# Kernel tuning notes

Measured on AMD Instinct MI355X. Metric: run time of the kernel, lower is better.

The kernel has to match this reference:

```python
import jax, jax.numpy as jnp
import numpy as np

CIN = 256
WINDOWS = (2, 4, 6)
LN_EPS = 1e-5


def _conv1x1(x, w, b):
    # x: (N,C,H,W), w: (O,C), b: (O,)
    return jnp.einsum('nchw,oc->nohw', x, w) + b[None, :, None, None]


def _pos_encoding(C, H, W):
    # Faithful to SinCosPositionalEncoding2D (incl. its w-major flatten + raw view)
    gw, gh = jnp.meshgrid(jnp.arange(W, dtype=jnp.float32),
                          jnp.arange(H, dtype=jnp.float32), indexing='ij')
    pd = C // 4
    omega = 1.0 / (10000.0 ** (jnp.arange(pd, dtype=jnp.float32) / pd))
    ow = gw.reshape(-1)[:, None] * omega[None, :]
    oh = gh.reshape(-1)[:, None] * omega[None, :]
    pe = jnp.concatenate([jnp.sin(ow), jnp.cos(ow), jnp.sin(oh), jnp.cos(oh)], axis=1)  # (W*H, C)
    return pe.reshape(1, C, H, W)  # raw row-major reinterpret, matching torch .view


def _unfold(x, kh, kw, sh, sw):
    # torch F.unfold semantics: (N,C,H,W) -> (N, C*kh*kw, L), L row-major over (oh, ow)
    N, C, H, W = x.shape
    oh = (H - kh) // sh + 1
    ow = (W - kw) // sw + 1
    ih = (jnp.arange(oh) * sh)[:, None] + jnp.arange(kh)[None, :]  # (oh,kh)
    iw = (jnp.arange(ow) * sw)[:, None] + jnp.arange(kw)[None, :]  # (ow,kw)
    p = x[:, :, ih[:, None, :, None], iw[None, :, None, :]]       # (N,C,oh,ow,kh,kw)
    return jnp.transpose(p, (0, 1, 4, 5, 2, 3)).reshape(N, C * kh * kw, oh * ow)


def _fold(p, H, W, kh, kw, sh, sw):
    # torch F.fold semantics: overlap-add scatter back to (N,C,H,W)
    N = p.shape[0]
    C = p.shape[1] // (kh * kw)
    oh = (H - kh) // sh + 1
    ow = (W - kw) // sw + 1
    p = jnp.transpose(p.reshape(N, C, kh, kw, oh, ow), (0, 1, 4, 5, 2, 3))  # (N,C,oh,ow,kh,kw)
    ih = (jnp.arange(oh) * sh)[:, None] + jnp.arange(kh)[None, :]
    iw = (jnp.arange(ow) * sw)[:, None] + jnp.arange(kw)[None, :]
    out = jnp.zeros((N, C, H, W), p.dtype)
    return out.at[:, :, ih[:, None, :, None], iw[None, :, None, :]].add(p)


def _psa(x, ch_wv_w, ch_wv_b, ch_wq_w, ch_wq_b, ch_wz_w, ch_wz_b, ln_g, ln_b,
         sp_wv_w, sp_wv_b, sp_wq_w, sp_wq_b):
    # Polarized Self-Attention (parallel), input (N,C,H',W')
    N, C, Hh, Ww = x.shape
    C2 = C // 2
    HW = Hh * Ww
    # channel-only branch
    wv = _conv1x1(x, ch_wv_w, ch_wv_b).reshape(N, C2, HW)
    wq = jax.nn.softmax(_conv1x1(x, ch_wq_w, ch_wq_b).reshape(N, HW), axis=-1)
    z = jnp.einsum('ncl,nl->nc', wv, wq)                       # (N, C2)
    wz = jnp.einsum('nc,oc->no', z, ch_wz_w) + ch_wz_b         # (N, C)
    m = wz.mean(-1, keepdims=True)
    v = ((wz - m) ** 2).mean(-1, keepdims=True)
    ch_w = jax.nn.sigmoid((wz - m) / jnp.sqrt(v + LN_EPS) * ln_g + ln_b)
    out_ch = x * ch_w[:, :, None, None]
    # spatial-only branch
    sv = _conv1x1(x, sp_wv_w, sp_wv_b).reshape(N, C2, HW)
    sq = jax.nn.softmax(_conv1x1(x, sp_wq_w, sp_wq_b).mean(axis=(2, 3)), axis=-1)  # (N,C2)
    sp_w = jax.nn.sigmoid(jnp.einsum('nc,ncl->nl', sq, sv)).reshape(N, 1, Hh, Ww)
    return out_ch + x * sp_w


def _forward(x, w_exp, b_exp, w_res, b_res, w_fus, b_fus,
             ch_wv_w, ch_wv_b, ch_wq_w, ch_wq_b, ch_wz_w, ch_wz_b, ln_g, ln_b,
             sp_wv_w, sp_wv_b, sp_wq_w, sp_wq_b):
    N, C, H, W = x.shape
    expx = _conv1x1(x, w_exp, b_exp)                 # (N, 3C, H, W)
    branches = jnp.split(expx, len(WINDOWS), axis=1)
    pos = _pos_encoding(C, H, W)
    outs = []
    for i, win in enumerate(WINDOWS):
        sh, sw = H // win, W // win
        kh, kw = sh + H % win, sw + W % win
        K = kh * kw
        u = _unfold(branches[i], kh, kw, sh, sw).reshape(N, C, win * win, K)
        pu = _unfold(pos, kh, kw, sh, sw).reshape(1, C, win * win, K)
        a = _psa(u + pu, ch_wv_w, ch_wv_b, ch_wq_w, ch_wq_b, ch_wz_w, ch_wz_b,
                 ln_g, ln_b, sp_wv_w, sp_wv_b, sp_wq_w, sp_wq_b)
        a = a.reshape(N, C * K, win * win)           # raw view, matching torch
        cnt = _fold(jnp.ones_like(a), H, W, kh, kw, sh, sw)
        f = _fold(a, H, W, kh, kw, sh, sw) / cnt
        outs.append(f)
    out = _conv1x1(jnp.concatenate(outs, axis=1) + expx, w_res, b_res) + x
    return _conv1x1(out, w_fus, b_fus)


def setup_inputs() -> dict:
    key = jax.random.key(0)
    ks = jax.random.split(key, 10)
    C, C2 = CIN, CIN // 2
    s = 0.02
    nrm = lambda k, shp: jax.random.normal(k, shp, jnp.float32) * s
    return {
        'x': jax.random.normal(ks[0], (8, C, 64, 64), jnp.float32),
        'w_exp': nrm(ks[1], (3 * C, C)), 'b_exp': jnp.zeros((3 * C,), jnp.float32),
        'w_res': nrm(ks[2], (C, 3 * C)), 'b_res': jnp.zeros((C,), jnp.float32),
        'w_fus': nrm(ks[3], (C, C)), 'b_fus': jnp.zeros((C,), jnp.float32),
        'ch_wv_w': nrm(ks[4], (C2, C)), 'ch_wv_b': jnp.zeros((C2,), jnp.float32),
        'ch_wq_w': nrm(ks[5], (1, C)), 'ch_wq_b': jnp.zeros((1,), jnp.float32),
        'ch_wz_w': nrm(ks[6], (C, C2)), 'ch_wz_b': jnp.zeros((C,), jnp.float32),
        'ln_g': jnp.ones((C,), jnp.float32), 'ln_b': jnp.zeros((C,), jnp.float32),
        'sp_wv_w': nrm(ks[7], (C2, C)), 'sp_wv_b': jnp.zeros((C2,), jnp.float32),
        'sp_wq_w': nrm(ks[8], (C2, C)), 'sp_wq_b': jnp.zeros((C2,), jnp.float32),
    }


def reference(x, w_exp, b_exp, w_res, b_res, w_fus, b_fus,
              ch_wv_w, ch_wv_b, ch_wq_w, ch_wq_b, ch_wz_w, ch_wz_b, ln_g, ln_b,
              sp_wv_w, sp_wv_b, sp_wq_w, sp_wq_b):
    return _forward(x, w_exp, b_exp, w_res, b_res, w_fus, b_fus,
                    ch_wv_w, ch_wv_b, ch_wq_w, ch_wq_b, ch_wz_w, ch_wz_b, ln_g, ln_b,
                    sp_wv_w, sp_wv_b, sp_wq_w, sp_wq_b)
```

## Files before the change

kernel.cpp:

```cpp
#include <hip/hip_runtime.h>
#include <cstddef>
#include <cstdint>


#define HW 4096
typedef unsigned short ushort_t;
typedef __attribute__((ext_vector_type(8))) short bf16x8;
typedef __attribute__((ext_vector_type(4))) float floatx4;

#define FMA4(acc, s, v) { acc.x = fmaf((s), (v).x, acc.x); acc.y = fmaf((s), (v).y, acc.y); \
                          acc.z = fmaf((s), (v).z, acc.z); acc.w = fmaf((s), (v).w, acc.w); }
#define SHRED4(v) { v.x += __shfl_down(v.x, 16, 64); v.y += __shfl_down(v.y, 16, 64); \
                    v.z += __shfl_down(v.z, 16, 64); v.w += __shfl_down(v.w, 16, 64); \
                    v.x += __shfl_down(v.x, 32, 64); v.y += __shfl_down(v.y, 32, 64); \
                    v.z += __shfl_down(v.z, 32, 64); v.w += __shfl_down(v.w, 32, 64); }
#define ADD4(a, b) { a.x += (b).x; a.y += (b).y; a.z += (b).z; a.w += (b).w; }

__device__ __forceinline__ ushort_t f2bf(float f) {
    unsigned u = __float_as_uint(f);
    u += 0x7FFF + ((u >> 16) & 1);
    return (ushort_t)(u >> 16);
}
__device__ __forceinline__ float bf2f(ushort_t h) {
    return __uint_as_float(((unsigned)h) << 16);
}

__device__ __forceinline__ int cnt1f(int y, int sh, int kh, int win) {
    int t = y - kh + sh;
    int lo = t > 0 ? t / sh : 0;
    int hi = min(win - 1, y / sh);
    return hi - lo + 1;
}

__device__ __forceinline__ float posval(int f) {
    int row = f >> 8, col = f & 255;
    int a = row >> 6, b = row & 63;
    int g = col >> 6, k = col & 63;
    float omega = expf(-(float)k * (9.2103403719761836f / 64.f));
    float arg = (g < 2 ? (float)a : (float)b) * omega;
    return (g & 1) ? cosf(arg) : sinf(arg);
}

__global__ __launch_bounds__(256) void prep_all(
    const float* __restrict__ x, const float* __restrict__ W_exp,
    const float* __restrict__ b_exp, const float* __restrict__ wq,
    const float* __restrict__ wq_b, const float* __restrict__ W_fus,
    const float* __restrict__ W_res, const float* __restrict__ b_res,
    const float* __restrict__ b_fus, const float* __restrict__ sp_wq_w,
    const float* __restrict__ ch_wv_w, const float* __restrict__ ch_wz_w,
    float* __restrict__ pos, float* __restrict__ posT,
    ushort_t* __restrict__ xbT, ushort_t* __restrict__ wexpb,
    float* __restrict__ g, float* __restrict__ c0out,
    ushort_t* __restrict__ Wcat, float* __restrict__ biasc,
    float* __restrict__ zeroreg,
    float* __restrict__ W_expT, float* __restrict__ swqT,
    float* __restrict__ chvT, float* __restrict__ chzT,
    float* __restrict__ xpa, float* __restrict__ xp6,
    float* __restrict__ ppa, float* __restrict__ pp6)
{
    __shared__ float smf[1184];
    __shared__ float wred[8];
    int b = blockIdx.x, tid = threadIdx.x;
    if (b < 4096) {
        int idx = b * 256 + tid;
        float pv = posval(idx);
        pos[idx] = pv;
        int p2 = idx >> 8, c2 = idx & 255;
        posT[idx] = posval(c2 * 4096 + p2);
        int p = ((b & 15) << 8) + tid;
        int y = p >> 6, xx = p & 63;
        float cf = (float)(cnt1f(y, 10, 14, 6) * cnt1f(xx, 10, 14, 6));
        float s1 = pv, s2 = cf * pv;
        #pragma unroll
        for (int d = 32; d; d >>= 1) {
            s1 += __shfl_down(s1, d, 64);
            s2 += __shfl_down(s2, d, 64);
        }
        if ((tid & 63) == 0) { wred[tid >> 6] = s1; wred[4 + (tid >> 6)] = s2; }
        __syncthreads();
        if (tid == 0) {
            int slot = (b & 15) * 256 + (b >> 4);
            ppa[slot] = wred[0] + wred[1] + wred[2] + wred[3];
            pp6[slot] = wred[4] + wred[5] + wred[6] + wred[7];
        }
    } else if (b < 12288) {
        int v = b - 4096;
        int p0 = (v & 127) * 32, c0 = ((v >> 7) & 7) * 32, n = v >> 10;
        int cc = tid >> 3, p4 = (tid & 7) * 4;
        const float* src = x + (((size_t)(n * 256 + c0 + cc)) << 12) + p0 + p4;
        float4 vv = *(const float4*)src;
        int pg = p0 + p4;
        int y = pg >> 6, xx = pg & 63;
        float cy = (float)cnt1f(y, 10, 14, 6);
        float s6 = cy * ((float)cnt1f(xx, 10, 14, 6) * vv.x
                       + (float)cnt1f(xx + 1, 10, 14, 6) * vv.y
                       + (float)cnt1f(xx + 2, 10, 14, 6) * vv.z
                       + (float)cnt1f(xx + 3, 10, 14, 6) * vv.w);
        float s = vv.x + vv.y + vv.z + vv.w;
        #pragma unroll
        for (int d = 4; d; d >>= 1) {
            s += __shfl_down(s, d, 8);
            s6 += __shfl_down(s6, d, 8);
        }
        if ((tid & 7) == 0) {
            int pblk = v & 127;
            xpa[pblk * 2048 + n * 256 + c0 + cc] = s;
            xp6[pblk * 2048 + n * 256 + c0 + cc] = s6;
        }
        smf[cc * 37 + p4] = vv.x; smf[cc * 37 + p4 + 1] = vv.y;
        smf[cc * 37 + p4 + 2] = vv.z; smf[cc * 37 + p4 + 3] = vv.w;
        __syncthreads();
        int pp = tid >> 3, c4 = (tid & 7) * 4;
        unsigned lo = (unsigned)f2bf(smf[c4 * 37 + pp]) | ((unsigned)f2bf(smf[(c4 + 1) * 37 + pp]) << 16);
        unsigned hi = (unsigned)f2bf(smf[(c4 + 2) * 37 + pp]) | ((unsigned)f2bf(smf[(c4 + 3) * 37 + pp]) << 16);
        *(uint2*)&xbT[(((size_t)(n << 12)) + p0 + pp) * 256 + c0 + c4] = make_uint2(lo, hi);
    } else if (b < 13056) {
        int i = (b - 12288) * 256 + tid;
        wexpb[i] = f2bf(W_exp[i]);
    } else if (b < 13059) {
        int i = b - 13056;
        float* wql = smf;
        float* red = smf + 256;
        wql[tid] = wq[tid];
        red[tid] = wq[tid] * b_exp[i * 256 + tid];
        __syncthreads();
        const float* Wb = W_exp + ((size_t)(i * 256)) * 256 + tid;
        float acc = 0.f;
        #pragma unroll 8
        for (int oc = 0; oc < 256; ++oc) acc = fmaf(wql[oc], Wb[(size_t)oc * 256], acc);
        g[i * 256 + tid] = acc;
        for (int s = 128; s > 0; s >>= 1) { if (tid < s) red[tid] += red[tid + s]; __syncthreads(); }
        if (tid == 0) c0out[i] = red[0] + wq_b[0];
    } else if (b < 13827) {
        int v = b - 13059;
        int o = v & 255, jb = v >> 8;
        float* wrow = smf;
        float* red = smf + 256;
        wrow[tid] = W_fus[o * 256 + tid];
        __syncthreads();
        int j = jb * 256 + tid;
        float acc = 0.f;
        #pragma unroll 8
        for (int c = 0; c < 256; ++c) acc = fmaf(wrow[c], W_res[(size_t)c * 768 + j], acc);
        Wcat[o * 1024 + 256 + j] = f2bf(acc);
        if (jb == 0) {
            Wcat[o * 1024 + tid] = f2bf(wrow[tid]);
            red[tid] = wrow[tid] * b_res[tid];
            __syncthreads();
            for (int s = 128; s > 0; s >>= 1) { if (tid < s) red[tid] += red[tid + s]; __syncthreads(); }
            if (tid == 0) biasc[o] = red[0] + b_fus[o];
        }
    } else if (b < 13875) {
        int i = (b - 13827) * 256 + tid;
        zeroreg[i] = 0.f;
    } else if (b < 14643) {
        int idx = (b - 13875) * 256 + tid;
        W_expT[(idx & 255) * 768 + (idx >> 8)] = W_exp[idx];
    } else if (b < 14771) {
        int idx = (b - 14643) * 256 + tid;
        swqT[(idx & 255) * 128 + (idx >> 8)] = sp_wq_w[idx];
    } else if (b < 14899) {
        int idx = (b - 14771) * 256 + tid;
        chvT[(idx & 255) * 128 + (idx >> 8)] = ch_wv_w[idx];
    } else {
        int idx = (b - 14899) * 256 + tid;
        chzT[(idx & 127) * 256 + (idx >> 7)] = ch_wz_w[idx];
    }
}

__global__ __launch_bounds__(512) void qdot_ubar(
    const float* __restrict__ x, const float* __restrict__ pos,
    const float* __restrict__ g, const float* __restrict__ c0in,
    const float* __restrict__ wq, float* __restrict__ qdot,
    const float* __restrict__ b_exp,
    const float* __restrict__ xpa, const float* __restrict__ xp6,
    const float* __restrict__ ppa, const float* __restrict__ pp6,
    const float* __restrict__ W_expT, float* __restrict__ ubar,
    float* __restrict__ qpm, float* __restrict__ qpz)
{
    int blk = blockIdx.x, tid = threadIdx.x;
    if (blk < 512) {
        int n = blk >> 6;
        int pq = tid & 15, cg = tid >> 4;
        int pb = blk & 63;
        int p = pb * 64 + pq * 4;
        __shared__ float gl[768];
        __shared__ float wql[256];
        __shared__ float4 wp[8][16][4];
        for (int k = tid; k < 768; k += 512) gl[k] = g[k];
        if (tid < 256) wql[tid] = wq[tid];
        __syncthreads();
        const float* xp = x + (((size_t)n) << 20) + p;
        const float* pp = pos + p;
        float4 a0 = make_float4(0.f, 0.f, 0.f, 0.f), a1 = a0, a2 = a0, ap = a0;
        #pragma unroll
        for (int c = cg * 8; c < cg * 8 + 8; ++c) {
            float4 xv = *(const float4*)(xp + ((size_t)c << 12));
            float4 pv = *(const float4*)(pp + ((size_t)c << 12));
            FMA4(a0, gl[c], xv);
            FMA4(a1, gl[256 + c], xv);
            FMA4(a2, gl[512 + c], xv);
            FMA4(ap, wql[c], pv);
        }
        SHRED4(a0); SHRED4(a1); SHRED4(a2); SHRED4(ap);
        int lane = tid & 63, w = tid >> 6;
        if (lane < 16) {
            wp[w][lane][0] = a0; wp[w][lane][1] = a1;
            wp[w][lane][2] = a2; wp[w][lane][3] = ap;
        }
        __syncthreads();
        if (tid < 16) {
            float4 s0 = make_float4(0.f, 0.f, 0.f, 0.f), s1 = s0, s2 = s0, sp = s0;
            #pragma unroll
            for (int w2 = 0; w2 < 8; ++w2) {
                ADD4(s0, wp[w2][tid][0]); ADD4(s1, wp[w2][tid][1]);
                ADD4(s2, wp[w2][tid][2]); ADD4(sp, wp[w2][tid][3]);
            }
            float c00 = c0in[0], c01 = c0in[1], c02 = c0in[2];
            float4 va, vb, vc;
            va.x = s0.x + sp.x + c00; va.y = s0.y + sp.y + c00;
            va.z = s0.z + sp.z + c00; va.w = s0.w + sp.w + c00;
            vb.x = s1.x + sp.x + c01; vb.y = s1.y + sp.y + c01;
            vb.z = s1.z + sp.z + c01; vb.w = s1.w + sp.w + c01;
            vc.x = s2.x + sp.x + c02; vc.y = s2.y + sp.y + c02;
            vc.z = s2.z + sp.z + c02; vc.w = s2.w + sp.w + c02;
            *(float4*)&qdot[((0 * 8 + n) << 12) + p] = va;
            *(float4*)&qdot[((1 * 8 + n) << 12) + p] = vb;
            *(float4*)&qdot[((2 * 8 + n) << 12) + p] = vc;
            int y = p >> 6, xx = p & 63;
            #pragma unroll
            for (int i = 0; i < 3; ++i) {
                int win = 2 * (i + 1), sh = 64 / win, kh = sh + 64 % win;
                float4 v = (i == 0) ? va : (i == 1) ? vb : vc;
                float cy = (float)cnt1f(y, sh, kh, win);
                float cf0 = cy * (float)cnt1f(xx, sh, kh, win);
                float cf1 = cy * (float)cnt1f(xx + 1, sh, kh, win);
                float cf2 = cy * (float)cnt1f(xx + 2, sh, kh, win);
                float cf3 = cy * (float)cnt1f(xx + 3, sh, kh, win);
                float m = fmaxf(fmaxf(v.x, v.y), fmaxf(v.z, v.w));
                #pragma unroll
                for (int d = 8; d; d >>= 1) m = fmaxf(m, __shfl_down(m, d, 16));
                m = __shfl(m, 0, 16);
                float z = cf0 * expf(v.x - m) + cf1 * expf(v.y - m)
                        + cf2 * expf(v.z - m) + cf3 * expf(v.w - m);
                #pragma unroll
                for (int d = 8; d; d >>= 1) z += __shfl_down(z, d, 16);
                if (tid == 0) {
                    int bidx = (i * 8 + n) * 64 + pb;
                    qpm[bidx] = m; qpz[bidx] = z;
                }
            }
        }
    } else {
        int v = blk - 512;
        int i = v >> 3, n = v & 7;
        __shared__ float xbl[256];
        if (tid < 256) {
            const float* xp_ = (i < 2) ? xpa : xp6;
            float s = 0.f;
            #pragma unroll 8
            for (int k = 0; k < 128; ++k) s += xp_[k * 2048 + n * 256 + tid];
            xbl[tid] = s;
        }
        __syncthreads();
        if (tid < 256) {
            const float* pp_ = (i < 2) ? ppa : pp6;
            float pb = 0.f;
            #pragma unroll
            for (int k = 0; k < 16; ++k) pb += pp_[k * 256 + tid];
            int win = 2 * (i + 1), sh = 64 / win, kh = sh + 64 % win;
            float Li = (float)(win * win * kh * kh);
            float acc = b_exp[i * 256 + tid] * Li + pb;
            const float* Wc = W_expT + i * 256 + tid;
            #pragma unroll 8
            for (int j = 0; j < 256; ++j) acc = fmaf(Wc[(size_t)j * 768], xbl[j], acc);
            ubar[(i * 8 + n) * 256 + tid] = acc;
        }
    }
}

__global__ __launch_bounds__(1024) void pass_b_h(
    const float* __restrict__ ubar_raw,
    const float* __restrict__ swqT, const float* __restrict__ sp_wq_b,
    const float* __restrict__ sp_wv_w, const float* __restrict__ sp_wv_b,
    const float* __restrict__ W_exp, const float* __restrict__ b_exp,
    const float* __restrict__ qpm, const float* __restrict__ qpz,
    float* __restrict__ Mn, float* __restrict__ invZn,
    float* __restrict__ w_eff, float* __restrict__ h, float* __restrict__ btot)
{
    int i = blockIdx.x, n = blockIdx.y, tid = threadIdx.x;
    int b = i * 8 + n;
    int win = 2 * (i + 1), sh = 64 / win, kh = sh + 64 % win;
    float invL = 1.f / (float)(win * win * kh * kh);
    __shared__ float ub[256];
    __shared__ float spq[128];
    __shared__ float we[256];
    __shared__ float ps[1024];
    __shared__ float red[256];
    if (tid < 64) {
        float mp = qpm[b * 64 + tid];
        float zp = qpz[b * 64 + tid];
        float mm = mp;
        #pragma unroll
        for (int d = 32; d; d >>= 1) mm = fmaxf(mm, __shfl_down(mm, d, 64));
        float M = __shfl(mm, 0, 64);
        float zz = zp * expf(mp - M);
        #pragma unroll
        for (int d = 32; d; d >>= 1) zz += __shfl_down(zz, d, 64);
        if (tid == 0) { Mn[b] = M; invZn[b] = 1.f / zz; }
    }
    if (tid < 256) ub[tid] = ubar_raw[b * 256 + tid] * invL;
    __syncthreads();
    {
        int q = tid & 127, s8 = tid >> 7;
        float a = 0.f;
        #pragma unroll 8
        for (int c = s8 * 32; c < s8 * 32 + 32; ++c) a = fmaf(swqT[c * 128 + q], ub[c], a);
        ps[tid] = a;
    }
    __syncthreads();
    float sl = 0.f;
    if (tid < 128) {
        float a = sp_wq_b[tid];
        #pragma unroll
        for (int k = 0; k < 8; ++k) a += ps[k * 128 + tid];
        sl = a;
        red[tid] = a;
    }
    __syncthreads();
    for (int s = 64; s > 0; s >>= 1) { if (tid < s) red[tid] = fmaxf(red[tid], red[tid + s]); __syncthreads(); }
    float m2 = red[0]; __syncthreads();
    float e = (tid < 128) ? expf(sl - m2) : 0.f;
    if (tid < 128) red[tid] = e;
    __syncthreads();
    for (int s = 64; s > 0; s >>= 1) { if (tid < s) red[tid] += red[tid + s]; __syncthreads(); }
    float S2 = red[0]; __syncthreads();
    if (tid < 128) spq[tid] = e / S2;
    __syncthreads();
    {
        int c = tid & 255, s4 = tid >> 8;
        float a = 0.f;
        #pragma unroll 8
        for (int q = s4 * 32; q < s4 * 32 + 32; ++q) a = fmaf(spq[q], sp_wv_w[q * 256 + c], a);
        ps[tid] = a;
    }
    __syncthreads();
    if (tid < 256) {
        float a = ps[tid] + ps[256 + tid] + ps[512 + tid] + ps[768 + tid];
        w_eff[b * 256 + tid] = a;
        we[tid] = a;
    }
    __syncthreads();
    {
        int c = tid & 255, s4 = tid >> 8;
        const float* Wb2 = W_exp + (size_t)i * 65536 + c;
        float a = 0.f;
        #pragma unroll 8
        for (int oc = s4 * 64; oc < s4 * 64 + 64; ++oc) a = fmaf(we[oc], Wb2[(size_t)oc * 256], a);
        ps[tid] = a;
    }
    __syncthreads();
    if (tid < 256) {
        h[b * 256 + tid] = ps[tid] + ps[256 + tid] + ps[512 + tid] + ps[768 + tid];
        red[tid] = we[tid] * b_exp[i * 256 + tid] + ((tid < 128) ? spq[tid] * sp_wv_b[tid] : 0.f);
    }
    __syncthreads();
    for (int s = 128; s > 0; s >>= 1) { if (tid < s) red[tid] += red[tid + s]; __syncthreads(); }
    if (tid == 0) btot[b] = red[0];
}

__global__ __launch_bounds__(512) void spw_t_xq(
    const float* __restrict__ x, const float* __restrict__ pos,
    const float* __restrict__ h, const float* __restrict__ weff,
    const float* __restrict__ qdot, const float* __restrict__ Mn,
    const float* __restrict__ invZn, const float* __restrict__ btot,
    const ushort_t* __restrict__ xbT, const float* __restrict__ posT,
    float* __restrict__ spw, float* __restrict__ xq, float* __restrict__ posq)
{
    int n = blockIdx.y, tid = threadIdx.x;
    int pq = tid & 15, cg = tid >> 4;
    int p0b = blockIdx.x * 64;
    int p = p0b + pq * 4;
    __shared__ float hl[768], wl[768];
    __shared__ float4 wp[8][16][3];
    __shared__ float tl[3][64];
    for (int k = tid; k < 768; k += 512) {
        int i = k >> 8, c = k & 255;
        hl[k] = h[(i * 8 + n) * 256 + c];
        wl[k] = weff[(i * 8 + n) * 256 + c];
    }
    __syncthreads();
    const float* xp = x + (((size_t)n) << 20) + p;
    const float* pp = pos + p;
    float4 a0 = make_float4(0.f, 0.f, 0.f, 0.f), a1 = a0, a2 = a0;
    #pragma unroll
    for (int c = cg * 8; c < cg * 8 + 8; ++c) {
        float4 xv = *(const float4*)(xp + ((size_t)c << 12));
        float4 pv = *(const float4*)(pp + ((size_t)c << 12));
        FMA4(a0, hl[c], xv);       FMA4(a0, wl[c], pv);
        FMA4(a1, hl[256 + c], xv); FMA4(a1, wl[256 + c], pv);
        FMA4(a2, hl[512 + c], xv); FMA4(a2, wl[512 + c], pv);
    }
    SHRED4(a0); SHRED4(a1); SHRED4(a2);
    int lane = tid & 63, w = tid >> 6;
    if (lane < 16) { wp[w][lane][0] = a0; wp[w][lane][1] = a1; wp[w][lane][2] = a2; }
    __syncthreads();
    if (tid < 16) {
        float4 s0 = make_float4(0.f, 0.f, 0.f, 0.f), s1 = s0, s2 = s0;
        #pragma unroll
        for (int w2 = 0; w2 < 8; ++w2) {
            ADD4(s0, wp[w2][tid][0]); ADD4(s1, wp[w2][tid][1]); ADD4(s2, wp[w2][tid][2]);
        }
        int y = p >> 6, xx = p & 63;
        #pragma unroll
        for (int i = 0; i < 3; ++i) {
            int b = i * 8 + n;
            int win = 2 * (i + 1), sh = 64 / win, kh = sh + 64 % win;
            float4 v = (i == 0) ? s0 : (i == 1) ? s1 : s2;
            float bt = btot[b];
            int idx = (b << 12) + p;
            float4 sv;
            sv.x = 1.f / (1.f + expf(-(v.x + bt)));
            sv.y = 1.f / (1.f + expf(-(v.y + bt)));
            sv.z = 1.f / (1.f + expf(-(v.z + bt)));
            sv.w = 1.f / (1.f + expf(-(v.w + bt)));
            *(float4*)&spw[idx] = sv;
            float cy = (float)cnt1f(y, sh, kh, win);
            float cf0 = cy * (float)cnt1f(xx, sh, kh, win);
            float cf1 = cy * (float)cnt1f(xx + 1, sh, kh, win);
            float cf2 = cy * (float)cnt1f(xx + 2, sh, kh, win);
            float cf3 = cy * (float)cnt1f(xx + 3, sh, kh, win);
            float4 qv = *(const float4*)&qdot[idx];
            float Mb = Mn[b], iZb = invZn[b];
            tl[i][pq * 4 + 0] = cf0 * expf(qv.x - Mb) * iZb;
            tl[i][pq * 4 + 1] = cf1 * expf(qv.y - Mb) * iZb;
            tl[i][pq * 4 + 2] = cf2 * expf(qv.z - Mb) * iZb;
            tl[i][pq * 4 + 3] = cf3 * expf(qv.w - Mb) * iZb;
        }
    }
    __syncthreads();
    int c = tid & 255;
    int half = tid >> 8;
    float s0 = 0.f, s1 = 0.f, s2 = 0.f;
    if (half == 0) {
        const ushort_t* xb = xbT + (((size_t)((n << 12) + p0b)) << 8) + c;
        #pragma unroll 4
        for (int pl = 0; pl < 64; ++pl) {
            float xv = bf2f(xb[(size_t)pl << 8]);
            s0 = fmaf(tl[0][pl], xv, s0);
            s1 = fmaf(tl[1][pl], xv, s1);
            s2 = fmaf(tl[2][pl], xv, s2);
        }
        atomicAdd(&xq[(0 * 8 + n) * 256 + c], s0);
        atomicAdd(&xq[(1 * 8 + n) * 256 + c], s1);
        atomicAdd(&xq[(2 * 8 + n) * 256 + c], s2);
    } else {
        const float* pt = posT + (((size_t)p0b) << 8) + c;
        #pragma unroll 4
        for (int pl = 0; pl < 64; ++pl) {
            float pv = pt[(size_t)pl << 8];
            s0 = fmaf(tl[0][pl], pv, s0);
            s1 = fmaf(tl[1][pl], pv, s1);
            s2 = fmaf(tl[2][pl], pv, s2);
        }
        atomicAdd(&posq[(0 * 8 + n) * 256 + c], s0);
        atomicAdd(&posq[(1 * 8 + n) * 256 + c], s1);
        atomicAdd(&posq[(2 * 8 + n) * 256 + c], s2);
    }
}

__global__ __launch_bounds__(1024) void pass_d_uq(
    const float* __restrict__ W_expT, const float* __restrict__ b_exp,
    const float* __restrict__ xq, const float* __restrict__ posq,
    const float* __restrict__ chvT, const float* __restrict__ ch_wv_b,
    const float* __restrict__ chzT, const float* __restrict__ ch_wz_b,
    const float* __restrict__ ln_g, const float* __restrict__ ln_b,
    float* __restrict__ ch_w)
{
    int i = blockIdx.x, n = blockIdx.y, tid = threadIdx.x;
    int b = i * 8 + n;
    __shared__ float xql[256];
    __shared__ float uql[256];
    __shared__ float zz[128];
    __shared__ float ps[1024];
    __shared__ float red[256];
    if (tid < 256) xql[tid] = xq[b * 256 + tid];
    __syncthreads();
    {
        int oc = tid & 255, s4 = tid >> 8;
        const float* Wc = W_expT + i * 256 + oc;
        float a = 0.f;
        #pragma unroll 8
        for (int cin = s4 * 64; cin < s4 * 64 + 64; ++cin) a = fmaf(Wc[(size_t)cin * 768], xql[cin], a);
        ps[tid] = a;
    }
    __syncthreads();
    if (tid < 256)
        uql[tid] = b_exp[i * 256 + tid] + posq[b * 256 + tid]
                 + ps[tid] + ps[256 + tid] + ps[512 + tid] + ps[768 + tid];
    __syncthreads();
    {
        int q = tid & 127, s8 = tid >> 7;
        float a = 0.f;
        #pragma unroll 8
        for (int c = s8 * 32; c < s8 * 32 + 32; ++c) a = fmaf(chvT[c * 128 + q], uql[c], a);
        ps[tid] = a;
    }
    __syncthreads();
    if (tid < 128) {
        float a = ch_wv_b[tid];
        #pragma unroll
        for (int k = 0; k < 8; ++k) a += ps[k * 128 + tid];
        zz[tid] = a;
    }
    __syncthreads();
    {
        int o = tid & 255, s4 = tid >> 8;
        float a = 0.f;
        #pragma unroll 8
        for (int c2 = s4 * 32; c2 < s4 * 32 + 32; ++c2) a = fmaf(chzT[c2 * 256 + o], zz[c2], a);
        ps[tid] = a;
    }
    __syncthreads();
    float wz = 0.f;
    if (tid < 256) {
        wz = ch_wz_b[tid] + ps[tid] + ps[256 + tid] + ps[512 + tid] + ps[768 + tid];
        red[tid] = wz;
    }
    __syncthreads();
    for (int s = 128; s > 0; s >>= 1) { if (tid < s) red[tid] += red[tid + s]; __syncthreads(); }
    float mean = red[0] * (1.f / 256.f); __syncthreads();
    float d = wz - mean;
    if (tid < 256) red[tid] = d * d;
    __syncthreads();
    for (int s = 128; s > 0; s >>= 1) { if (tid < s) red[tid] += red[tid + s]; __syncthreads(); }
    float var = red[0] * (1.f / 256.f);
    if (tid < 256) {
        float xn = d / sqrtf(var + 1e-5f);
        ch_w[b * 256 + tid] = 1.f / (1.f + expf(-(xn * ln_g[tid] + ln_b[tid])));
    }
}

__global__ __launch_bounds__(256) void gemm_expT(
    const ushort_t* __restrict__ Wb, const ushort_t* __restrict__ XT,
    const float* __restrict__ bias, const float* __restrict__ posT,
    const float* __restrict__ chw, const float* __restrict__ spw,
    ushort_t* __restrict__ OutT)
{
    __shared__ ushort_t SM[10240];
    ushort_t* As = SM;
    ushort_t* Bs = SM + 5120;
    int n = blockIdx.z;
    int p0 = blockIdx.x * 128;
    int o0 = blockIdx.y * 128;
    int t = threadIdx.x;
    int lane = t & 63, wave = t >> 6;
    int wm = (wave & 1) * 64, wn = (wave >> 1) * 64;
    int lr = lane & 15, lk = (lane >> 4) * 8;
    int ar = t >> 2, ac = (t & 3) * 8;
    const ushort_t* A0 = Wb + (size_t)(o0 + ar) * 256 + ac;
    const ushort_t* A1 = Wb + (size_t)(o0 + ar + 64) * 256 + ac;
    const ushort_t* B0 = XT + (((size_t)(n << 12)) + p0 + ar) * 256 + ac;
    const ushort_t* B1 = XT + (((size_t)(n << 12)) + p0 + ar + 64) * 256 + ac;
    floatx4 acc[4][4] = {};
    for (int k0 = 0; k0 < 256; k0 += 32) {
        uint4 a0 = *(const uint4*)(A0 + k0);
        uint4 a1 = *(const uint4*)(A1 + k0);
        uint4 b0 = *(const uint4*)(B0 + k0);
        uint4 b1 = *(const uint4*)(B1 + k0);
        __syncthreads();
        *(uint4*)&As[ar * 40 + ac] = a0;
        *(uint4*)&As[(ar + 64) * 40 + ac] = a1;
        *(uint4*)&Bs[ar * 40 + ac] = b0;
        *(uint4*)&Bs[(ar + 64) * 40 + ac] = b1;
        __syncthreads();
        bf16x8 af[4], bfr[4];
        #pragma unroll
        for (int mi = 0; mi < 4; ++mi)
            af[mi] = *(const bf16x8*)&As[(wm + mi * 16 + lr) * 40 + lk];
        #pragma unroll
        for (int ni = 0; ni < 4; ++ni)
            bfr[ni] = *(const bf16x8*)&Bs[(wn + ni * 16 + lr) * 40 + lk];
        #pragma unroll
        for (int mi = 0; mi < 4; ++mi)
            #pragma unroll
            for (int ni = 0; ni < 4; ++ni)
                acc[mi][ni] = __builtin_amdgcn_mfma_f32_16x16x32_bf16(
                    af[mi], bfr[ni], acc[mi][ni], 0, 0, 0);
    }
    int col = lane & 15, rb = (lane >> 4) * 4;
    int ibr = o0 >> 8;
    int bi = ibr * 8 + n;
    #pragma unroll
    for (int r = 0; r < 2; ++r) {
        __syncthreads();
        if (wm == r * 64) {
            #pragma unroll
            for (int mi = 0; mi < 4; ++mi) {
                int o_loc = mi * 16 + rb;
                float4 bo = *(const float4*)&bias[o0 + r * 64 + o_loc];
                #pragma unroll
                for (int ni = 0; ni < 4; ++ni) {
                    int prow = wn + ni * 16 + col;
                    floatx4 v = acc[mi][ni];
                    unsigned lo = (unsigned)f2bf(v[0] + bo.x) | ((unsigned)f2bf(v[1] + bo.y) << 16);
                    unsigned hi = (unsigned)f2bf(v[2] + bo.z) | ((unsigned)f2bf(v[3] + bo.w) << 16);
                    *(uint2*)&SM[prow * 72 + o_loc] = make_uint2(lo, hi);
                }
            }
        }
        __syncthreads();
        #pragma unroll
        for (int it = 0; it < 4; ++it) {
            int slot = it * 256 + t;
            int pl = slot >> 3, j = (slot & 7) * 8;
            uint4 raw = *(const uint4*)&SM[pl * 72 + j];
            float e0 = bf2f((ushort_t)(raw.x & 0xFFFF)), e1 = bf2f((ushort_t)(raw.x >> 16));
            float e2 = bf2f((ushort_t)(raw.y & 0xFFFF)), e3 = bf2f((ushort_t)(raw.y >> 16));
            float e4 = bf2f((ushort_t)(raw.z & 0xFFFF)), e5 = bf2f((ushort_t)(raw.z >> 16));
            float e6 = bf2f((ushort_t)(raw.w & 0xFFFF)), e7 = bf2f((ushort_t)(raw.w >> 16));
            int p = p0 + pl;
            int cbase = (o0 & 255) + r * 64 + j;
            float s = spw[(bi << 12) + p];
            float4 q0 = *(const float4*)&posT[p * 256 + cbase];
            float4 q1 = *(const float4*)&posT[p * 256 + cbase + 4];
            float4 w0 = *(const float4*)&chw[bi * 256 + cbase];
            float4 w1 = *(const float4*)&chw[bi * 256 + cbase + 4];
            float r0 = e0 + (e0 + q0.x) * (w0.x + s);
            float r1 = e1 + (e1 + q0.y) * (w0.y + s);
            float r2 = e2 + (e2 + q0.z) * (w0.z + s);
            float r3 = e3 + (e3 + q0.w) * (w0.w + s);
            float r4 = e4 + (e4 + q1.x) * (w1.x + s);
            float r5 = e5 + (e5 + q1.y) * (w1.y + s);
            float r6 = e6 + (e6 + q1.z) * (w1.z + s);
            float r7 = e7 + (e7 + q1.w) * (w1.w + s);
            uint4 outv;
            outv.x = (unsigned)f2bf(r0) | ((unsigned)f2bf(r1) << 16);
            outv.y = (unsigned)f2bf(r2) | ((unsigned)f2bf(r3) << 16);
            outv.z = (unsigned)f2bf(r4) | ((unsigned)f2bf(r5) << 16);
            outv.w = (unsigned)f2bf(r6) | ((unsigned)f2bf(r7) << 16);
            *(uint4*)&OutT[(((size_t)(n << 12)) + p) * 768 + o0 + r * 64 + j] = outv;
        }
    }
}

__global__ __launch_bounds__(256) void gemm_out(
    const ushort_t* __restrict__ Wcat, const ushort_t* __restrict__ XT,
    const ushort_t* __restrict__ CT, const float* __restrict__ biasc,
    float* __restrict__ Out)
{
    __shared__ ushort_t As[128 * 40];
    __shared__ ushort_t Bs[128 * 40];
    int n = blockIdx.z;
    int p0 = blockIdx.x * 128;
    int o0 = blockIdx.y * 128;
    int t = threadIdx.x;
    int lane = t & 63, wave = t >> 6;
    int wm = (wave & 1) * 64, wn = (wave >> 1) * 64;
    int lr = lane & 15, lk = (lane >> 4) * 8;
    int ar = t >> 2, ac = (t & 3) * 8;
    const ushort_t* A0 = Wcat + (size_t)(o0 + ar) * 1024 + ac;
    const ushort_t* A1 = Wcat + (size_t)(o0 + ar + 64) * 1024 + ac;
    const ushort_t* BX0 = XT + (((size_t)(n << 12)) + p0 + ar) * 256 + ac;
    const ushort_t* BX1 = XT + (((size_t)(n << 12)) + p0 + ar + 64) * 256 + ac;
    const ushort_t* BC0 = CT + (((size_t)(n << 12)) + p0 + ar) * 768 + ac;
    const ushort_t* BC1 = CT + (((size_t)(n << 12)) + p0 + ar + 64) * 768 + ac;
    floatx4 acc[4][4] = {};
    for (int k0 = 0; k0 < 1024; k0 += 32) {
        const ushort_t* pb0 = (k0 < 256) ? (BX0 + k0) : (BC0 + (k0 - 256));
        const ushort_t* pb1 = (k0 < 256) ? (BX1 + k0) : (BC1 + (k0 - 256));
        uint4 a0 = *(const uint4*)(A0 + k0);
        uint4 a1 = *(const uint4*)(A1 + k0);
        uint4 b0 = *(const uint4*)pb0;
        uint4 b1 = *(const uint4*)pb1;
        __syncthreads();
        *(uint4*)&As[ar * 40 + ac] = a0;
        *(uint4*)&As[(ar + 64) * 40 + ac] = a1;
        *(uint4*)&Bs[ar * 40 + ac] = b0;
        *(uint4*)&Bs[(ar + 64) * 40 + ac] = b1;
        __syncthreads();
        bf16x8 af[4], bfr[4];
        #pragma unroll
        for (int mi = 0; mi < 4; ++mi)
            af[mi] = *(const bf16x8*)&As[(wm + mi * 16 + lr) * 40 + lk];
        #pragma unroll
        for (int ni = 0; ni < 4; ++ni)
            bfr[ni] = *(const bf16x8*)&Bs[(wn + ni * 16 + lr) * 40 + lk];
        #pragma unroll
        for (int mi = 0; mi < 4; ++mi)
            #pragma unroll
            for (int ni = 0; ni < 4; ++ni)
                acc[mi][ni] = __builtin_amdgcn_mfma_f32_16x16x32_bf16(
                    af[mi], bfr[ni], acc[mi][ni], 0, 0, 0);
    }
    int col = lane & 15, rb = (lane >> 4) * 4;
    #pragma unroll
    for (int mi = 0; mi < 4; ++mi) {
        int o = o0 + wm + mi * 16 + rb;
        float4 bo = *(const float4*)&biasc[o];
        #pragma unroll
        for (int r = 0; r < 4; ++r) {
            float br = (r == 0) ? bo.x : (r == 1) ? bo.y : (r == 2) ? bo.z : bo.w;
            #pragma unroll
            for (int ni = 0; ni < 4; ++ni) {
                int p = p0 + wn + ni * 16 + col;
                Out[(((size_t)(n * 256 + o + r)) << 12) + p] = acc[mi][ni][r] + br;
            }
        }
    }
}

extern "C" void kernel_launch(void* const* d_in, const int* in_sizes, int n_in,
                              void* d_out, int out_size, void* d_ws, size_t ws_size,
                              hipStream_t stream) {
    const float* x        = (const float*)d_in[0];
    const float* w_exp    = (const float*)d_in[1];
    const float* b_exp    = (const float*)d_in[2];
    const float* w_res    = (const float*)d_in[3];
    const float* b_res    = (const float*)d_in[4];
    const float* w_fus    = (const float*)d_in[5];
    const float* b_fus    = (const float*)d_in[6];
    const float* ch_wv_w  = (const float*)d_in[7];
    const float* ch_wv_b  = (const float*)d_in[8];
    const float* ch_wq_w  = (const float*)d_in[9];
    const float* ch_wq_b  = (const float*)d_in[10];
    const float* ch_wz_w  = (const float*)d_in[11];
    const float* ch_wz_b  = (const float*)d_in[12];
    const float* ln_g     = (const float*)d_in[13];
    const float* ln_b     = (const float*)d_in[14];
    const float* sp_wv_w  = (const float*)d_in[15];
    const float* sp_wv_b  = (const float*)d_in[16];
    const float* sp_wq_w  = (const float*)d_in[17];
    const float* sp_wq_b  = (const float*)d_in[18];
    float* out = (float*)d_out;
    float* ws  = (float*)d_ws;

    float*    pos   = ws + 0;
    float*    posT  = ws + 1048576;
    ushort_t* xbT   = (ushort_t*)(ws + 2097152);
    ushort_t* exT   = (ushort_t*)(ws + 6291456);
    ushort_t* wexpb = (ushort_t*)(ws + 18874368);
    ushort_t* Wcat  = (ushort_t*)(ws + 18972672);
    float*    qdot  = ws + 19103744;
    float*    spw   = ws + 19300352;
    float*    g     = ws + 19398656;
    float*    c0v   = ws + 19399424;
    float*    ubar  = ws + 19399428;
    float*    Mn    = ws + 19410180;
    float*    iZ    = ws + 19410204;
    float*    weff  = ws + 19410228;
    float*    btot  = ws + 19416372;
    float*    hb    = ws + 19416396;
    float*    xq    = ws + 19422540;
    float*    posq  = ws + 19428684;
    float*    chw   = ws + 19434828;
    float*    biasc = ws + 19440972;
    float*    W_expT = ws + 19441228;
    float*    swqT   = ws + 19637836;
    float*    chvT   = ws + 19670604;
    float*    chzT   = ws + 19703372;
    float*    xpa    = ws + 19736140;
    float*    xp6    = ws + 19998284;
    float*    ppa    = ws + 20260428;
    float*    pp6    = ws + 20264524;
    float*    qpm    = ws + 20268620;
    float*    qpz    = ws + 20270156;

    prep_all<<<15027, 256, 0, stream>>>(x, w_exp, b_exp, ch_wq_w, ch_wq_b,
                                        w_fus, w_res, b_res, b_fus,
                                        sp_wq_w, ch_wv_w, ch_wz_w,
                                        pos, posT, xbT, wexpb, g, c0v,
                                        Wcat, biasc, xq,
                                        W_expT, swqT, chvT, chzT,
                                        xpa, xp6, ppa, pp6);
    qdot_ubar<<<536, 512, 0, stream>>>(x, pos, g, c0v, ch_wq_w, qdot,
                                       b_exp, xpa, xp6, ppa, pp6, W_expT, ubar,
                                       qpm, qpz);
    pass_b_h<<<dim3(3, 8), 1024, 0, stream>>>(ubar, swqT, sp_wq_b,
                                              sp_wv_w, sp_wv_b, w_exp, b_exp,
                                              qpm, qpz,
                                              Mn, iZ, weff, hb, btot);
    spw_t_xq<<<dim3(64, 8), 512, 0, stream>>>(x, pos, hb, weff, qdot, Mn, iZ,
                                              btot, xbT, posT, spw, xq, posq);
    pass_d_uq<<<dim3(3, 8), 1024, 0, stream>>>(W_expT, b_exp, xq, posq,
                                               chvT, ch_wv_b, chzT, ch_wz_b,
                                               ln_g, ln_b, chw);
    gemm_expT<<<dim3(32, 6, 8), 256, 0, stream>>>(wexpb, xbT, b_exp, posT, chw, spw, exT);
    gemm_out<<<dim3(32, 2, 8), 256, 0, stream>>>(Wcat, xbT, exT, biasc, out);
}
```

Baseline: 260.1 us.

## Reuse register-held x/pos tiles for weighted pooled sums instead of reloading transposed copies

The kernel now keeps the x and pos float4 values loaded for the first reduction in registers. It reuses them for the second, token-weighted channel reduction, using 16-lane shuffle reductions and atomics per channel. This removes the second pass over the bf16-transposed x and the transposed pos arrays, cutting global memory traffic. The trade-offs are higher register pressure, more shuffle work and more atomics, and the pooled x sum now uses fp32 x instead of bf16 x.

```diff
diff --git a/kernel.cpp b/kernel.cpp
--- a/kernel.cpp
+++ b/kernel.cpp
@@ -392,14 +392,16 @@
     __syncthreads();
     const float* xp = x + (((size_t)n) << 20) + p;
     const float* pp = pos + p;
+    float4 xv[8], pv[8];
     float4 a0 = make_float4(0.f, 0.f, 0.f, 0.f), a1 = a0, a2 = a0;
     #pragma unroll
-    for (int c = cg * 8; c < cg * 8 + 8; ++c) {
-        float4 xv = *(const float4*)(xp + ((size_t)c << 12));
-        float4 pv = *(const float4*)(pp + ((size_t)c << 12));
-        FMA4(a0, hl[c], xv);       FMA4(a0, wl[c], pv);
-        FMA4(a1, hl[256 + c], xv); FMA4(a1, wl[256 + c], pv);
-        FMA4(a2, hl[512 + c], xv); FMA4(a2, wl[512 + c], pv);
+    for (int k = 0; k < 8; ++k) {
+        int c = cg * 8 + k;
+        xv[k] = *(const float4*)(xp + ((size_t)c << 12));
+        pv[k] = *(const float4*)(pp + ((size_t)c << 12));
+        FMA4(a0, hl[c], xv[k]);       FMA4(a0, wl[c], pv[k]);
+        FMA4(a1, hl[256 + c], xv[k]); FMA4(a1, wl[256 + c], pv[k]);
+        FMA4(a2, hl[512 + c], xv[k]); FMA4(a2, wl[512 + c], pv[k]);
     }
     SHRED4(a0); SHRED4(a1); SHRED4(a2);
     int lane = tid & 63, w = tid >> 6;
@@ -439,33 +441,24 @@
         }
     }
     __syncthreads();
-    int c = tid & 255;
-    int half = tid >> 8;
-    float s0 = 0.f, s1 = 0.f, s2 = 0.f;
-    if (half == 0) {
-        const ushort_t* xb = xbT + (((size_t)((n << 12) + p0b)) << 8) + c;
-        #pragma unroll 4
-        for (int pl = 0; pl < 64; ++pl) {
-            float xv = bf2f(xb[(size_t)pl << 8]);
-            s0 = fmaf(tl[0][pl], xv, s0);
-            s1 = fmaf(tl[1][pl], xv, s1);
-            s2 = fmaf(tl[2][pl], xv, s2);
-        }
-        atomicAdd(&xq[(0 * 8 + n) * 256 + c], s0);
-        atomicAdd(&xq[(1 * 8 + n) * 256 + c], s1);
-        atomicAdd(&xq[(2 * 8 + n) * 256 + c], s2);
-    } else {
-        const float* pt = posT + (((size_t)p0b) << 8) + c;
-        #pragma unroll 4
-        for (int pl = 0; pl < 64; ++pl) {
-            float pv = pt[(size_t)pl << 8];
-            s0 = fmaf(tl[0][pl], pv, s0);
-            s1 = fmaf(tl[1][pl], pv, s1);
-            s2 = fmaf(tl[2][pl], pv, s2);
-        }
-        atomicAdd(&posq[(0 * 8 + n) * 256 + c], s0);
-        atomicAdd(&posq[(1 * 8 + n) * 256 + c], s1);
-        atomicAdd(&posq[(2 * 8 + n) * 256 + c], s2);
+    #pragma unroll
+    for (int i = 0; i < 3; ++i) {
+        float t0 = tl[i][pq * 4 + 0], t1 = tl[i][pq * 4 + 1];
+        float t2 = tl[i][pq * 4 + 2], t3 = tl[i][pq * 4 + 3];
+        #pragma unroll
+        for (int k = 0; k < 8; ++k) {
+            float sx = t0 * xv[k].x + t1 * xv[k].y + t2 * xv[k].z + t3 * xv[k].w;
+            float sp = t0 * pv[k].x + t1 * pv[k].y + t2 * pv[k].z + t3 * pv[k].w;
+            #pragma unroll
+            for (int d = 8; d; d >>= 1) {
+                sx += __shfl_down(sx, d, 16);
+                sp += __shfl_down(sp, d, 16);
+            }
+            if (pq == 0) {
+                atomicAdd(&xq[(i * 8 + n) * 256 + cg * 8 + k], sx);
+                atomicAdd(&posq[(i * 8 + n) * 256 + cg * 8 + k], sp);
+            }
+        }
     }
 }
 
```

Result: slower. 319.3 us (+22.7%).
